# Kernel optimization log

Hardware: AMD Instinct MI355X
Metric: run time of the kernel (lower is better)

## Reference

```python
import jax, jax.numpy as jnp
import numpy as np

C = 512        # concept_num
D = 256        # input_dim / embedding_dim
H = 512        # msg_hidden_dim
M = 256        # msg_output_dim
OH = 512       # hidden_dim
T = 2          # edge_type_num
E = C * (C - 1)  # fully-connected graph without self-loops = 261632


def _glorot(key, shape, fan_in):
    return jax.random.normal(key, shape, jnp.float32) / np.sqrt(fan_in).astype(np.float32)


def setup_inputs() -> dict:
    key = jax.random.key(0)
    ks = jax.random.split(key, 12)
    inputs = jax.random.normal(ks[0], (C, D), jnp.float32)
    rel_type = jax.random.uniform(ks[1], (E, T), jnp.float32)
    send_idx = jax.random.randint(ks[2], (E,), 0, C, jnp.int32)
    rec_idx = jax.random.randint(ks[3], (E,), 0, C, jnp.int32)
    # per-edge-type message MLP params, stacked over type dim
    W1 = _glorot(ks[4], (T, 2 * D, H), 2 * D)
    b1 = jnp.zeros((T, H), jnp.float32)
    W2 = _glorot(ks[5], (T, H, M), H)
    b2 = jnp.zeros((T, M), jnp.float32)
    # output MLP params
    Wo1 = _glorot(ks[6], (M, OH), M)
    bo1 = jnp.zeros((OH,), jnp.float32)
    Wo2 = _glorot(ks[7], (OH, OH), OH)
    bo2 = jnp.zeros((OH,), jnp.float32)
    Wo3 = _glorot(ks[8], (OH, D), OH)
    bo3 = jnp.zeros((D,), jnp.float32)
    return {"inputs": inputs, "rel_type": rel_type, "W1": W1, "b1": b1,
            "W2": W2, "b2": b2, "Wo1": Wo1, "bo1": bo1, "Wo2": Wo2,
            "bo2": bo2, "Wo3": Wo3, "bo3": bo3,
            "send_idx": send_idx, "rec_idx": rec_idx}


def reference(inputs, rel_type, W1, b1, W2, b2, Wo1, bo1, Wo2, bo2, Wo3, bo3,
              send_idx, rec_idx):
    # node2edge: one-hot sparse matmul == index gather
    senders = jnp.take(inputs, send_idx, axis=0)      # [E, D]
    receivers = jnp.take(inputs, rec_idx, axis=0)     # [E, D]
    pre_msg = jnp.concatenate([senders, receivers], axis=-1)  # [E, 2D]
    # per-edge-type MLPs, weighted-summed by rel_type (dropout=0 / eval mode)
    all_msgs = jnp.zeros((pre_msg.shape[0], M), jnp.float32)
    for i in range(T):
        msg = jax.nn.relu(pre_msg @ W1[i] + b1[i])    # [E, H]
        msg = jax.nn.relu(msg @ W2[i] + b2[i])        # [E, M]
        all_msgs = all_msgs + msg * rel_type[:, i:i + 1]
    # edge2node: transposed one-hot sparse matmul == scatter-add over receivers
    agg_msgs = jax.ops.segment_sum(all_msgs, rec_idx, num_segments=inputs.shape[0])  # [C, M]
    pred = jax.nn.relu(agg_msgs @ Wo1 + bo1)
    pred = jax.nn.relu(pred @ Wo2 + bo2)
    return pred @ Wo3 + bo3                           # [C, D]
```

## Files before the change

kernel.cpp:

```cpp
#include <hip/hip_runtime.h>

#define C_N   512
#define E_N   261632
#define CAP   768

typedef _Float16 f16;
typedef _Float16 f16x8_t __attribute__((ext_vector_type(8)));
typedef float    f32x16_t __attribute__((ext_vector_type(16)));

__global__ __launch_bounds__(256) void k_prep_all(
    const float* __restrict__ inputs, const float* __restrict__ W1,
    const float* __restrict__ b1, const float* __restrict__ W2,
    const float* __restrict__ Wo1, const float* __restrict__ Wo2, const float* __restrict__ Wo3,
    f16* __restrict__ SA, f16* __restrict__ RB, f16* __restrict__ W2p,
    f16* __restrict__ Wo1p, f16* __restrict__ Wo2p, f16* __restrict__ Wo3p,
    int* __restrict__ cnt)
{
  __shared__ f16 wt[2][256][18];
  int bid = blockIdx.x;
  int tid = threadIdx.x;
  if (bid < 64) {
    int lane = tid & 63, w = tid >> 6;
    int hlf = lane >> 5, l31 = lane & 31;
    int br = bid & 7, bc = (bid >> 3) & 1, mi = bid >> 4;
    int t = mi >> 1, half = mi & 1;
    const float* Wsrc = W1 + (size_t)t * 512 * 512 + (size_t)half * 256 * 512;

    f32x16_t acc[2][2];
    #pragma unroll
    for (int rt = 0; rt < 2; rt++)
      #pragma unroll
      for (int ctl = 0; ctl < 2; ctl++)
        #pragma unroll
        for (int r = 0; r < 16; r++) acc[rt][ctl][r] = 0.f;

    #pragma unroll
    for (int i = 0; i < 4; i++) {
      int idx = tid + i * 256;
      int k = idx >> 6, n4 = idx & 63;
      float4 v = *(const float4*)&Wsrc[(size_t)k * 512 + bc * 256 + n4 * 4];
      wt[0][n4 * 4 + 0][k] = (f16)v.x;
      wt[0][n4 * 4 + 1][k] = (f16)v.y;
      wt[0][n4 * 4 + 2][k] = (f16)v.z;
      wt[0][n4 * 4 + 3][k] = (f16)v.w;
    }

    for (int kc = 0; kc < 16; kc++) {
      __syncthreads();
      if (kc + 1 < 16) {
        int b = (kc + 1) & 1;
        #pragma unroll
        for (int i = 0; i < 4; i++) {
          int idx = tid + i * 256;
          int k = idx >> 6, n4 = idx & 63;
          float4 v = *(const float4*)&Wsrc[(size_t)((kc + 1) * 16 + k) * 512 + bc * 256 + n4 * 4];
          wt[b][n4 * 4 + 0][k] = (f16)v.x;
          wt[b][n4 * 4 + 1][k] = (f16)v.y;
          wt[b][n4 * 4 + 2][k] = (f16)v.z;
          wt[b][n4 * 4 + 3][k] = (f16)v.w;
        }
      }
      f16x8_t af[2];
      #pragma unroll
      for (int rt = 0; rt < 2; rt++) {
        const float4* p = (const float4*)&inputs[(size_t)(br * 64 + rt * 32 + l31) * 256 + kc * 16 + hlf * 8];
        float4 u0 = p[0], u1 = p[1];
        af[rt] = (f16x8_t){(f16)u0.x, (f16)u0.y, (f16)u0.z, (f16)u0.w,
                           (f16)u1.x, (f16)u1.y, (f16)u1.z, (f16)u1.w};
      }
      int b = kc & 1;
      #pragma unroll
      for (int ctl = 0; ctl < 2; ctl++) {
        int n = (2 * w + ctl) * 32 + l31;
        f16x8_t bfr = *(const f16x8_t*)&wt[b][n][hlf * 8];
        #pragma unroll
        for (int rt = 0; rt < 2; rt++)
          acc[rt][ctl] = __builtin_amdgcn_mfma_f32_32x32x16_f16(af[rt], bfr, acc[rt][ctl], 0, 0, 0);
      }
    }
    f16* dst = (half == 0) ? SA : RB;
    #pragma unroll
    for (int ctl = 0; ctl < 2; ctl++) {
      int col = bc * 256 + (2 * w + ctl) * 32 + l31;
      float bias = (half == 1) ? b1[t * 512 + col] : 0.f;
      #pragma unroll
      for (int rt = 0; rt < 2; rt++)
        #pragma unroll
        for (int r = 0; r < 16; r++) {
          int row = br * 64 + rt * 32 + (r & 3) + 8 * (r >> 2) + 4 * hlf;
          dst[((size_t)(t * 512 + row)) * 512 + col] = (f16)(acc[rt][ctl][r] + bias);
        }
    }
  } else if (bid < 192) {
    int gid  = (bid - 64) * 256 + tid;
    int lane = gid & 63;
    int ct   = (gid >> 6) & 7;
    int kc   = (gid >> 9) & 31;
    int t    = gid >> 14;
    int n    = ct * 32 + (lane & 31);
    int k0   = kc * 16 + (lane >> 5) * 8;
    const float* src = W2 + (size_t)t * 512 * 256;
    f16x8_t v;
    #pragma unroll
    for (int j = 0; j < 8; j++) v[j] = (f16)src[(size_t)(k0 + j) * 256 + n];
    *(f16x8_t*)(W2p + (size_t)gid * 8) = v;
  } else if (bid < 256) {
    int gid  = (bid - 192) * 256 + tid;
    int lane = gid & 63;
    int ct   = (gid >> 6) & 15;
    int kc   = gid >> 10;
    int n    = ct * 32 + (lane & 31);
    int k0   = kc * 16 + (lane >> 5) * 8;
    f16x8_t v;
    #pragma unroll
    for (int j = 0; j < 8; j++) v[j] = (f16)Wo1[(size_t)(k0 + j) * 512 + n];
    *(f16x8_t*)(Wo1p + (size_t)gid * 8) = v;
  } else if (bid < 384) {
    int gid  = (bid - 256) * 256 + tid;
    int lane = gid & 63;
    int ct   = (gid >> 6) & 15;
    int kc   = gid >> 10;
    int n    = ct * 32 + (lane & 31);
    int k0   = kc * 16 + (lane >> 5) * 8;
    f16x8_t v;
    #pragma unroll
    for (int j = 0; j < 8; j++) v[j] = (f16)Wo2[(size_t)(k0 + j) * 512 + n];
    *(f16x8_t*)(Wo2p + (size_t)gid * 8) = v;
  } else if (bid < 448) {
    int gid  = (bid - 384) * 256 + tid;
    int lane = gid & 63;
    int ct   = (gid >> 6) & 7;
    int kc   = gid >> 9;
    int n    = ct * 32 + (lane & 31);
    int k0   = kc * 16 + (lane >> 5) * 8;
    f16x8_t v;
    #pragma unroll
    for (int j = 0; j < 8; j++) v[j] = (f16)Wo3[(size_t)(k0 + j) * 256 + n];
    *(f16x8_t*)(Wo3p + (size_t)gid * 8) = v;
  } else {
    for (int i = tid; i < 512 * 16; i += 256) cnt[i] = 0;
  }
}

__global__ __launch_bounds__(1024) void k_scatter_d(const int* __restrict__ rec,
    const int* __restrict__ send, const float* __restrict__ rel,
    int* __restrict__ cnt, uint2* __restrict__ smeta)
{
  __shared__ int lh[512];
  __shared__ int lb[512];
  int b = blockIdx.x;
  int e0 = b * (E_N / 64);
  if (threadIdx.x < 512) lh[threadIdx.x] = 0;
  __syncthreads();
  for (int i = threadIdx.x; i < E_N / 64; i += 1024)
    atomicAdd(&lh[rec[e0 + i]], 1);
  __syncthreads();
  if (threadIdx.x < 512) {
    int c = lh[threadIdx.x];
    lb[threadIdx.x] = c ? atomicAdd(&cnt[threadIdx.x * 16], c) : 0;
    lh[threadIdx.x] = 0;
  }
  __syncthreads();
  for (int i = threadIdx.x; i < E_N / 64; i += 1024) {
    int e = e0 + i;
    int r = rec[e];
    int p = r * CAP + lb[r] + atomicAdd(&lh[r], 1);
    f16 r0 = (f16)rel[2 * (size_t)e];
    f16 r1 = (f16)rel[2 * (size_t)e + 1];
    unsigned pk = ((unsigned)__builtin_bit_cast(unsigned short, r1) << 16)
                |  (unsigned)__builtin_bit_cast(unsigned short, r0);
    smeta[p] = make_uint2((unsigned)send[e], pk);
  }
}

#define H1S2 264

__global__ __launch_bounds__(512, 4) void k_edges(
    const f16* __restrict__ SA, const f16* __restrict__ RB,
    const f16* __restrict__ W2p, const float* __restrict__ b2,
    const uint2* __restrict__ smeta, const int* __restrict__ cnt,
    float* __restrict__ agg)
{
  __shared__ f16   h1[128 * H1S2];
  __shared__ f16   rbs[2][512];
  __shared__ float b2s[2][256];
  __shared__ float aggL[256];
  __shared__ float relv2[2][128][2];
  __shared__ int   sends2[2][128];

  int c    = blockIdx.x;
  int tid  = threadIdx.x;
  int lane = tid & 63;
  int w    = tid >> 6;
  int hlf  = lane >> 5;
  int l31  = lane & 31;
  int q5   = tid & 31;
  int rb0  = tid >> 5;

  if (tid < 128) {
    int t = tid >> 6, qq = tid & 63;
    *(f16x8_t*)&rbs[t][qq * 8] = *(const f16x8_t*)&RB[((size_t)(t * 512 + c)) * 512 + qq * 8];
  }
  if (tid < 256) aggL[tid] = 0.0f;
  { int t = (tid >> 8) & 1, col = tid & 255; b2s[t][col] = b2[t * 256 + col]; }

  int s0 = c * CAP;
  int s1 = s0 + cnt[c * 16];
  int nt = (s1 - s0 + 127) >> 7;

  if (nt > 0 && tid < 128) {
    int pos = s0 + tid;
    if (pos < s1) {
      uint2 m = smeta[pos];
      sends2[0][tid] = (int)m.x;
      relv2[0][tid][0] = (float)__builtin_bit_cast(f16, (unsigned short)(m.y & 0xffffu));
      relv2[0][tid][1] = (float)__builtin_bit_cast(f16, (unsigned short)(m.y >> 16));
    } else {
      sends2[0][tid] = 0; relv2[0][tid][0] = 0.f; relv2[0][tid][1] = 0.f;
    }
  }
  __syncthreads();

  f16x8_t g[8];
  const f16x8_t* SAc = (const f16x8_t*)SA;
  const f16x8_t* Bp  = (const f16x8_t*)W2p;
  f32x16_t acc[4];

  if (nt > 0) {
    #pragma unroll
    for (int j = 0; j < 8; j++)
      g[j] = SAc[(size_t)sends2[0][rb0 + 16 * j] * 64 + q5];
  }

  for (int ph = 0; ph < 4 * nt; ph++) {
    int ti  = ph >> 2;
    int t   = (ph >> 1) & 1;
    int kh  = ph & 1;
    int cb  = ti & 1;
    int nb  = cb ^ 1;
    bool more = (ti + 1 < nt);

    {
      f16x8_t rbq = *(const f16x8_t*)&rbs[t][(kh * 32 + q5) * 8];
      #pragma unroll
      for (int j = 0; j < 8; j++) {
        int row = rb0 + 16 * j;
        f16x8_t hv;
        #pragma unroll
        for (int e = 0; e < 8; e++) {
          f16 v = (f16)(g[j][e] + rbq[e]);
          hv[e] = (v > (f16)0.0f) ? v : (f16)0.0f;
        }
        *(f16x8_t*)&h1[row * H1S2 + q5 * 8] = hv;
      }
    }
    __syncthreads();

    if (t == 0 && kh == 0 && more && tid < 128) {
      int pos = s0 + (ti + 1) * 128 + tid;
      if (pos < s1) {
        uint2 m = smeta[pos];
        sends2[nb][tid] = (int)m.x;
        relv2[nb][tid][0] = (float)__builtin_bit_cast(f16, (unsigned short)(m.y & 0xffffu));
        relv2[nb][tid][1] = (float)__builtin_bit_cast(f16, (unsigned short)(m.y >> 16));
      } else {
        sends2[nb][tid] = 0; relv2[nb][tid][0] = 0.f; relv2[nb][tid][1] = 0.f;
      }
    }

    if (kh == 0) {
      #pragma unroll
      for (int rt = 0; rt < 4; rt++)
        #pragma unroll
        for (int r = 0; r < 16; r++) acc[rt][r] = 0.f;
    }

    f16x8_t bb[2];
    bb[0] = Bp[(size_t)(((t * 32 + kh * 16 + 0) * 8 + w) * 64 + lane)];
    bb[1] = Bp[(size_t)(((t * 32 + kh * 16 + 1) * 8 + w) * 64 + lane)];

    if (kh == 0) {
      #pragma unroll
      for (int j = 0; j < 8; j++)
        g[j] = SAc[(size_t)(t * 512 + sends2[cb][rb0 + 16 * j]) * 64 + 32 + q5];
    } else if (t == 0) {
      #pragma unroll
      for (int j = 0; j < 8; j++)
        g[j] = SAc[(size_t)(512 + sends2[cb][rb0 + 16 * j]) * 64 + q5];
    } else if (more) {
      #pragma unroll
      for (int j = 0; j < 8; j++)
        g[j] = SAc[(size_t)sends2[nb][rb0 + 16 * j] * 64 + q5];
    }

    for (int kc = 0; kc < 16; kc++) {
      int pb = kc & 1;
      #pragma unroll
      for (int rt = 0; rt < 4; rt++) {
        f16x8_t af = *(const f16x8_t*)&h1[(rt * 32 + l31) * H1S2 + kc * 16 + hlf * 8];
        acc[rt] = __builtin_amdgcn_mfma_f32_32x32x16_f16(af, bb[pb], acc[rt], 0, 0, 0);
      }
      if (kc + 2 < 16)
        bb[pb] = Bp[(size_t)(((t * 32 + kh * 16 + kc + 2) * 8 + w) * 64 + lane)];
    }

    if (kh == 1) {
      int col = w * 32 + l31;
      float b2c = b2s[t][col];
      float csum = 0.0f;
      #pragma unroll
      for (int rt = 0; rt < 4; rt++)
        #pragma unroll
        for (int r = 0; r < 16; r++) {
          int row = rt * 32 + (r & 3) + 8 * (r >> 2) + 4 * hlf;
          float v = fmaxf(acc[rt][r] + b2c, 0.0f);
          csum += v * relv2[cb][row][t];
        }
      csum += __shfl_xor(csum, 32, 64);
      if (hlf == 0) aggL[col] += csum;
    }
    __syncthreads();
  }

  if (tid < 256) agg[(size_t)c * 256 + tid] = aggL[tid];
}

#define HOS 520

__global__ __launch_bounds__(512, 1) void k_omlp(const float* __restrict__ agg,
    const f16* __restrict__ Wo1p, const float* __restrict__ bo1,
    const f16* __restrict__ Wo2p, const float* __restrict__ bo2,
    const f16* __restrict__ Wo3p, const float* __restrict__ bo3,
    float* __restrict__ out)
{
  __shared__ f16 hL1[64 * HOS];
  __shared__ f16 hL2[64 * HOS];
  int tid = threadIdx.x, lane = tid & 63, w = tid >> 6;
  int hlf = lane >> 5, l31 = lane & 31;
  int br = blockIdx.x;

  {
    f32x16_t acc[2][2];
    #pragma unroll
    for (int rt = 0; rt < 2; rt++)
      #pragma unroll
      for (int ctl = 0; ctl < 2; ctl++)
        #pragma unroll
        for (int r = 0; r < 16; r++) acc[rt][ctl][r] = 0.f;
    for (int kc = 0; kc < 16; kc++) {
      f16x8_t af[2];
      #pragma unroll
      for (int rt = 0; rt < 2; rt++) {
        const float4* p = (const float4*)&agg[(size_t)(br * 64 + rt * 32 + l31) * 256 + kc * 16 + hlf * 8];
        float4 u0 = p[0], u1 = p[1];
        af[rt] = (f16x8_t){(f16)u0.x, (f16)u0.y, (f16)u0.z, (f16)u0.w,
                           (f16)u1.x, (f16)u1.y, (f16)u1.z, (f16)u1.w};
      }
      #pragma unroll
      for (int ctl = 0; ctl < 2; ctl++) {
        int ct = 2 * w + ctl;
        f16x8_t bfr = *(const f16x8_t*)&Wo1p[((size_t)(kc * 16 + ct) * 64 + lane) * 8];
        #pragma unroll
        for (int rt = 0; rt < 2; rt++)
          acc[rt][ctl] = __builtin_amdgcn_mfma_f32_32x32x16_f16(af[rt], bfr, acc[rt][ctl], 0, 0, 0);
      }
    }
    #pragma unroll
    for (int ctl = 0; ctl < 2; ctl++) {
      int col = (2 * w + ctl) * 32 + l31;
      float bias = bo1[col];
      #pragma unroll
      for (int rt = 0; rt < 2; rt++)
        #pragma unroll
        for (int r = 0; r < 16; r++) {
          int row = rt * 32 + (r & 3) + 8 * (r >> 2) + 4 * hlf;
          hL1[row * HOS + col] = (f16)fmaxf(acc[rt][ctl][r] + bias, 0.f);
        }
    }
  }
  __syncthreads();

  {
    f32x16_t acc[2][2];
    #pragma unroll
    for (int rt = 0; rt < 2; rt++)
      #pragma unroll
      for (int ctl = 0; ctl < 2; ctl++)
        #pragma unroll
        for (int r = 0; r < 16; r++) acc[rt][ctl][r] = 0.f;
    for (int kc = 0; kc < 32; kc++) {
      f16x8_t af[2];
      #pragma unroll
      for (int rt = 0; rt < 2; rt++)
        af[rt] = *(const f16x8_t*)&hL1[(rt * 32 + l31) * HOS + kc * 16 + hlf * 8];
      #pragma unroll
      for (int ctl = 0; ctl < 2; ctl++) {
        int ct = 2 * w + ctl;
        f16x8_t bfr = *(const f16x8_t*)&Wo2p[((size_t)(kc * 16 + ct) * 64 + lane) * 8];
        #pragma unroll
        for (int rt = 0; rt < 2; rt++)
          acc[rt][ctl] = __builtin_amdgcn_mfma_f32_32x32x16_f16(af[rt], bfr, acc[rt][ctl], 0, 0, 0);
      }
    }
    #pragma unroll
    for (int ctl = 0; ctl < 2; ctl++) {
      int col = (2 * w + ctl) * 32 + l31;
      float bias = bo2[col];
      #pragma unroll
      for (int rt = 0; rt < 2; rt++)
        #pragma unroll
        for (int r = 0; r < 16; r++) {
          int row = rt * 32 + (r & 3) + 8 * (r >> 2) + 4 * hlf;
          hL2[row * HOS + col] = (f16)fmaxf(acc[rt][ctl][r] + bias, 0.f);
        }
    }
  }
  __syncthreads();

  {
    f32x16_t acc[2];
    #pragma unroll
    for (int rt = 0; rt < 2; rt++)
      #pragma unroll
      for (int r = 0; r < 16; r++) acc[rt][r] = 0.f;
    for (int kc = 0; kc < 32; kc++) {
      f16x8_t bfr = *(const f16x8_t*)&Wo3p[((size_t)(kc * 8 + w) * 64 + lane) * 8];
      #pragma unroll
      for (int rt = 0; rt < 2; rt++) {
        f16x8_t af = *(const f16x8_t*)&hL2[(rt * 32 + l31) * HOS + kc * 16 + hlf * 8];
        acc[rt] = __builtin_amdgcn_mfma_f32_32x32x16_f16(af, bfr, acc[rt], 0, 0, 0);
      }
    }
    int col = w * 32 + l31;
    float bias = bo3[col];
    #pragma unroll
    for (int rt = 0; rt < 2; rt++)
      #pragma unroll
      for (int r = 0; r < 16; r++) {
        int row = br * 64 + rt * 32 + (r & 3) + 8 * (r >> 2) + 4 * hlf;
        out[(size_t)row * 256 + col] = acc[rt][r] + bias;
      }
  }
}

extern "C" void kernel_launch(void* const* d_in, const int* in_sizes, int n_in,
                              void* d_out, int out_size, void* d_ws, size_t ws_size,
                              hipStream_t stream)
{
  (void)in_sizes; (void)n_in; (void)out_size; (void)ws_size;
  const float* inputs = (const float*)d_in[0];
  const float* rel    = (const float*)d_in[1];
  const float* W1     = (const float*)d_in[2];
  const float* b1     = (const float*)d_in[3];
  const float* W2     = (const float*)d_in[4];
  const float* b2     = (const float*)d_in[5];
  const float* Wo1    = (const float*)d_in[6];
  const float* bo1    = (const float*)d_in[7];
  const float* Wo2    = (const float*)d_in[8];
  const float* bo2    = (const float*)d_in[9];
  const float* Wo3    = (const float*)d_in[10];
  const float* bo3    = (const float*)d_in[11];
  const int* send_idx = (const int*)d_in[12];
  const int* rec_idx  = (const int*)d_in[13];
  float* out = (float*)d_out;

  char* ws = (char*)d_ws;
  f16*    SA    = (f16*)   (ws);
  f16*    RB    = (f16*)   (ws + (1024u << 10));
  f16*    W2p   = (f16*)   (ws + (2048u << 10));
  float*  agg   = (float*) (ws + (2560u << 10));
  int*    cnt   = (int*)   (ws + (3072u << 10));
  f16*    Wo1p  = (f16*)   (ws + (3136u << 10));
  f16*    Wo2p  = (f16*)   (ws + (3392u << 10));
  f16*    Wo3p  = (f16*)   (ws + (3904u << 10));
  uint2*  smeta = (uint2*) (ws + (4160u << 10));

  k_prep_all <<<dim3(449), dim3(256),  0, stream>>>(inputs, W1, b1, W2, Wo1, Wo2, Wo3,
                                                    SA, RB, W2p, Wo1p, Wo2p, Wo3p, cnt);
  k_scatter_d<<<dim3(64),  dim3(1024), 0, stream>>>(rec_idx, send_idx, rel, cnt, smeta);
  k_edges    <<<dim3(512), dim3(512),  0, stream>>>(SA, RB, W2p, b2, smeta, cnt, agg);
  k_omlp     <<<dim3(8),   dim3(512),  0, stream>>>(agg, Wo1p, bo1, Wo2p, bo2, Wo3p, bo3, out);
}
```

Before: 309.5 us.

## Split edge tiles across a 2D grid with atomic aggregation, widen scatter and output MLP grids

The edge kernel now launches one block per (receiver, 128-edge tile) on a 512x5 grid instead of looping over every tile of a receiver inside one block. Partial sums are combined with atomicAdd into agg, which the prep kernel now zeroes in an extra block. This spreads work over more blocks and removes imbalance from receivers with many edges, at the cost of reloading RB and b2 per tile, extra atomics, and empty blocks that exit early. The scatter kernel uses 128 blocks of 512 threads, and the output MLP uses 16 blocks of 32 rows each, to raise parallelism in both.

After: 298.9 us, median of 2. -3.4%, faster.

```diff
diff --git a/kernel.cpp b/kernel.cpp
--- a/kernel.cpp
+++ b/kernel.cpp
@@ -14,7 +14,7 @@
     const float* __restrict__ Wo1, const float* __restrict__ Wo2, const float* __restrict__ Wo3,
     f16* __restrict__ SA, f16* __restrict__ RB, f16* __restrict__ W2p,
     f16* __restrict__ Wo1p, f16* __restrict__ Wo2p, f16* __restrict__ Wo3p,
-    int* __restrict__ cnt)
+    int* __restrict__ cnt, float* __restrict__ agg)
 {
   __shared__ f16 wt[2][256][18];
   int bid = blockIdx.x;
@@ -137,31 +137,34 @@
     #pragma unroll
     for (int j = 0; j < 8; j++) v[j] = (f16)Wo3[(size_t)(k0 + j) * 256 + n];
     *(f16x8_t*)(Wo3p + (size_t)gid * 8) = v;
+  } else if (bid == 448) {
+    for (int i = tid; i < 512 * 16; i += 256) cnt[i] = 0;
   } else {
-    for (int i = tid; i < 512 * 16; i += 256) cnt[i] = 0;
+    float4* a4 = (float4*)agg;
+    for (int i = tid; i < 512 * 64; i += 256) a4[i] = make_float4(0.f, 0.f, 0.f, 0.f);
   }
 }
 
-__global__ __launch_bounds__(1024) void k_scatter_d(const int* __restrict__ rec,
+__global__ __launch_bounds__(512) void k_scatter_d(const int* __restrict__ rec,
     const int* __restrict__ send, const float* __restrict__ rel,
     int* __restrict__ cnt, uint2* __restrict__ smeta)
 {
   __shared__ int lh[512];
   __shared__ int lb[512];
   int b = blockIdx.x;
-  int e0 = b * (E_N / 64);
-  if (threadIdx.x < 512) lh[threadIdx.x] = 0;
-  __syncthreads();
-  for (int i = threadIdx.x; i < E_N / 64; i += 1024)
+  int e0 = b * (E_N / 128);
+  lh[threadIdx.x] = 0;
+  __syncthreads();
+  for (int i = threadIdx.x; i < E_N / 128; i += 512)
     atomicAdd(&lh[rec[e0 + i]], 1);
   __syncthreads();
-  if (threadIdx.x < 512) {
+  {
     int c = lh[threadIdx.x];
     lb[threadIdx.x] = c ? atomicAdd(&cnt[threadIdx.x * 16], c) : 0;
     lh[threadIdx.x] = 0;
   }
   __syncthreads();
-  for (int i = threadIdx.x; i < E_N / 64; i += 1024) {
+  for (int i = threadIdx.x; i < E_N / 128; i += 512) {
     int e = e0 + i;
     int r = rec[e];
     int p = r * CAP + lb[r] + atomicAdd(&lh[r], 1);
@@ -185,10 +188,14 @@
   __shared__ f16   rbs[2][512];
   __shared__ float b2s[2][256];
   __shared__ float aggL[256];
-  __shared__ float relv2[2][128][2];
-  __shared__ int   sends2[2][128];
-
-  int c    = blockIdx.x;
+  __shared__ float relv[128][2];
+  __shared__ int   sends[128];
+
+  int c   = blockIdx.x;
+  int ti  = blockIdx.y;
+  int n_c = cnt[c * 16];
+  if (ti * 128 >= n_c) return;
+
   int tid  = threadIdx.x;
   int lane = tid & 63;
   int w    = tid >> 6;
@@ -204,19 +211,17 @@
   if (tid < 256) aggL[tid] = 0.0f;
   { int t = (tid >> 8) & 1, col = tid & 255; b2s[t][col] = b2[t * 256 + col]; }
 
-  int s0 = c * CAP;
-  int s1 = s0 + cnt[c * 16];
-  int nt = (s1 - s0 + 127) >> 7;
-
-  if (nt > 0 && tid < 128) {
-    int pos = s0 + tid;
-    if (pos < s1) {
-      uint2 m = smeta[pos];
-      sends2[0][tid] = (int)m.x;
-      relv2[0][tid][0] = (float)__builtin_bit_cast(f16, (unsigned short)(m.y & 0xffffu));
-      relv2[0][tid][1] = (float)__builtin_bit_cast(f16, (unsigned short)(m.y >> 16));
+  int s0 = c * CAP + ti * 128;
+  int nv = n_c - ti * 128; if (nv > 128) nv = 128;
+
+  if (tid < 128) {
+    if (tid < nv) {
+      uint2 m = smeta[s0 + tid];
+      sends[tid] = (int)m.x;
+      relv[tid][0] = (float)__builtin_bit_cast(f16, (unsigned short)(m.y & 0xffffu));
+      relv[tid][1] = (float)__builtin_bit_cast(f16, (unsigned short)(m.y >> 16));
     } else {
-      sends2[0][tid] = 0; relv2[0][tid][0] = 0.f; relv2[0][tid][1] = 0.f;
+      sends[tid] = 0; relv[tid][0] = 0.f; relv[tid][1] = 0.f;
     }
   }
   __syncthreads();
@@ -226,19 +231,13 @@
   const f16x8_t* Bp  = (const f16x8_t*)W2p;
   f32x16_t acc[4];
 
-  if (nt > 0) {
-    #pragma unroll
-    for (int j = 0; j < 8; j++)
-      g[j] = SAc[(size_t)sends2[0][rb0 + 16 * j] * 64 + q5];
-  }
-
-  for (int ph = 0; ph < 4 * nt; ph++) {
-    int ti  = ph >> 2;
-    int t   = (ph >> 1) & 1;
-    int kh  = ph & 1;
-    int cb  = ti & 1;
-    int nb  = cb ^ 1;
-    bool more = (ti + 1 < nt);
+  #pragma unroll
+  for (int j = 0; j < 8; j++)
+    g[j] = SAc[(size_t)sends[rb0 + 16 * j] * 64 + q5];
+
+  for (int ph = 0; ph < 4; ph++) {
+    int t  = ph >> 1;
+    int kh = ph & 1;
 
     {
       f16x8_t rbq = *(const f16x8_t*)&rbs[t][(kh * 32 + q5) * 8];
@@ -256,18 +255,6 @@
     }
     __syncthreads();
 
-    if (t == 0 && kh == 0 && more && tid < 128) {
-      int pos = s0 + (ti + 1) * 128 + tid;
-      if (pos < s1) {
-        uint2 m = smeta[pos];
-        sends2[nb][tid] = (int)m.x;
-        relv2[nb][tid][0] = (float)__builtin_bit_cast(f16, (unsigned short)(m.y & 0xffffu));
-        relv2[nb][tid][1] = (float)__builtin_bit_cast(f16, (unsigned short)(m.y >> 16));
-      } else {
-        sends2[nb][tid] = 0; relv2[nb][tid][0] = 0.f; relv2[nb][tid][1] = 0.f;
-      }
-    }
-
     if (kh == 0) {
       #pragma unroll
       for (int rt = 0; rt < 4; rt++)
@@ -279,18 +266,12 @@
     bb[0] = Bp[(size_t)(((t * 32 + kh * 16 + 0) * 8 + w) * 64 + lane)];
     bb[1] = Bp[(size_t)(((t * 32 + kh * 16 + 1) * 8 + w) * 64 + lane)];
 
-    if (kh == 0) {
+    if (ph < 3) {
+      int tn  = (ph + 1) >> 1;
+      int khn = (ph + 1) & 1;
       #pragma unroll
       for (int j = 0; j < 8; j++)
-        g[j] = SAc[(size_t)(t * 512 + sends2[cb][rb0 + 16 * j]) * 64 + 32 + q5];
-    } else if (t == 0) {
-      #pragma unroll
-      for (int j = 0; j < 8; j++)
-        g[j] = SAc[(size_t)(512 + sends2[cb][rb0 + 16 * j]) * 64 + q5];
-    } else if (more) {
-      #pragma unroll
-      for (int j = 0; j < 8; j++)
-        g[j] = SAc[(size_t)sends2[nb][rb0 + 16 * j] * 64 + q5];
+        g[j] = SAc[(size_t)(tn * 512 + sends[rb0 + 16 * j]) * 64 + khn * 32 + q5];
     }
 
     for (int kc = 0; kc < 16; kc++) {
@@ -314,7 +295,7 @@
         for (int r = 0; r < 16; r++) {
           int row = rt * 32 + (r & 3) + 8 * (r >> 2) + 4 * hlf;
           float v = fmaxf(acc[rt][r] + b2c, 0.0f);
-          csum += v * relv2[cb][row][t];
+          csum += v * relv[row][t];
         }
       csum += __shfl_xor(csum, 32, 64);
       if (hlf == 0) aggL[col] += csum;
@@ -322,7 +303,7 @@
     __syncthreads();
   }
 
-  if (tid < 256) agg[(size_t)c * 256 + tid] = aggL[tid];
+  if (tid < 256) atomicAdd(&agg[(size_t)c * 256 + tid], aggL[tid]);
 }
 
 #define HOS 520
@@ -333,36 +314,28 @@
     const f16* __restrict__ Wo3p, const float* __restrict__ bo3,
     float* __restrict__ out)
 {
-  __shared__ f16 hL1[64 * HOS];
-  __shared__ f16 hL2[64 * HOS];
+  __shared__ f16 hL1[32 * HOS];
+  __shared__ f16 hL2[32 * HOS];
   int tid = threadIdx.x, lane = tid & 63, w = tid >> 6;
   int hlf = lane >> 5, l31 = lane & 31;
   int br = blockIdx.x;
 
   {
-    f32x16_t acc[2][2];
-    #pragma unroll
-    for (int rt = 0; rt < 2; rt++)
-      #pragma unroll
-      for (int ctl = 0; ctl < 2; ctl++)
-        #pragma unroll
-        for (int r = 0; r < 16; r++) acc[rt][ctl][r] = 0.f;
+    f32x16_t acc[2];
+    #pragma unroll
+    for (int ctl = 0; ctl < 2; ctl++)
+      #pragma unroll
+      for (int r = 0; r < 16; r++) acc[ctl][r] = 0.f;
     for (int kc = 0; kc < 16; kc++) {
-      f16x8_t af[2];
-      #pragma unroll
-      for (int rt = 0; rt < 2; rt++) {
-        const float4* p = (const float4*)&agg[(size_t)(br * 64 + rt * 32 + l31) * 256 + kc * 16 + hlf * 8];
-        float4 u0 = p[0], u1 = p[1];
-        af[rt] = (f16x8_t){(f16)u0.x, (f16)u0.y, (f16)u0.z, (f16)u0.w,
-                           (f16)u1.x, (f16)u1.y, (f16)u1.z, (f16)u1.w};
-      }
+      const float4* p = (const float4*)&agg[(size_t)(br * 32 + l31) * 256 + kc * 16 + hlf * 8];
+      float4 u0 = p[0], u1 = p[1];
+      f16x8_t af = (f16x8_t){(f16)u0.x, (f16)u0.y, (f16)u0.z, (f16)u0.w,
+                             (f16)u1.x, (f16)u1.y, (f16)u1.z, (f16)u1.w};
       #pragma unroll
       for (int ctl = 0; ctl < 2; ctl++) {
         int ct = 2 * w + ctl;
         f16x8_t bfr = *(const f16x8_t*)&Wo1p[((size_t)(kc * 16 + ct) * 64 + lane) * 8];
-        #pragma unroll
-        for (int rt = 0; rt < 2; rt++)
-          acc[rt][ctl] = __builtin_amdgcn_mfma_f32_32x32x16_f16(af[rt], bfr, acc[rt][ctl], 0, 0, 0);
+        acc[ctl] = __builtin_amdgcn_mfma_f32_32x32x16_f16(af, bfr, acc[ctl], 0, 0, 0);
       }
     }
     #pragma unroll
@@ -370,36 +343,27 @@
       int col = (2 * w + ctl) * 32 + l31;
       float bias = bo1[col];
       #pragma unroll
-      for (int rt = 0; rt < 2; rt++)
-        #pragma unroll
-        for (int r = 0; r < 16; r++) {
-          int row = rt * 32 + (r & 3) + 8 * (r >> 2) + 4 * hlf;
-          hL1[row * HOS + col] = (f16)fmaxf(acc[rt][ctl][r] + bias, 0.f);
-        }
+      for (int r = 0; r < 16; r++) {
+        int row = (r & 3) + 8 * (r >> 2) + 4 * hlf;
+        hL1[row * HOS + col] = (f16)fmaxf(acc[ctl][r] + bias, 0.f);
+      }
     }
   }
   __syncthreads();
 
   {
-    f32x16_t acc[2][2];
-    #pragma unroll
-    for (int rt = 0; rt < 2; rt++)
-      #pragma unroll
-      for (int ctl = 0; ctl < 2; ctl++)
-        #pragma unroll
-        for (int r = 0; r < 16; r++) acc[rt][ctl][r] = 0.f;
+    f32x16_t acc[2];
+    #pragma unroll
+    for (int ctl = 0; ctl < 2; ctl++)
+      #pragma unroll
+      for (int r = 0; r < 16; r++) acc[ctl][r] = 0.f;
     for (int kc = 0; kc < 32; kc++) {
-      f16x8_t af[2];
-      #pragma unroll
-      for (int rt = 0; rt < 2; rt++)
-        af[rt] = *(const f16x8_t*)&hL1[(rt * 32 + l31) * HOS + kc * 16 + hlf * 8];
+      f16x8_t af = *(const f16x8_t*)&hL1[l31 * HOS + kc * 16 + hlf * 8];
       #pragma unroll
       for (int ctl = 0; ctl < 2; ctl++) {
         int ct = 2 * w + ctl;
         f16x8_t bfr = *(const f16x8_t*)&Wo2p[((size_t)(kc * 16 + ct) * 64 + lane) * 8];
-        #pragma unroll
-        for (int rt = 0; rt < 2; rt++)
-          acc[rt][ctl] = __builtin_amdgcn_mfma_f32_32x32x16_f16(af[rt], bfr, acc[rt][ctl], 0, 0, 0);
+        acc[ctl] = __builtin_amdgcn_mfma_f32_32x32x16_f16(af, bfr, acc[ctl], 0, 0, 0);
       }
     }
     #pragma unroll
@@ -407,39 +371,30 @@
       int col = (2 * w + ctl) * 32 + l31;
       float bias = bo2[col];
       #pragma unroll
-      for (int rt = 0; rt < 2; rt++)
-        #pragma unroll
-        for (int r = 0; r < 16; r++) {
-          int row = rt * 32 + (r & 3) + 8 * (r >> 2) + 4 * hlf;
-          hL2[row * HOS + col] = (f16)fmaxf(acc[rt][ctl][r] + bias, 0.f);
-        }
+      for (int r = 0; r < 16; r++) {
+        int row = (r & 3) + 8 * (r >> 2) + 4 * hlf;
+        hL2[row * HOS + col] = (f16)fmaxf(acc[ctl][r] + bias, 0.f);
+      }
     }
   }
   __syncthreads();
 
   {
-    f32x16_t acc[2];
-    #pragma unroll
-    for (int rt = 0; rt < 2; rt++)
-      #pragma unroll
-      for (int r = 0; r < 16; r++) acc[rt][r] = 0.f;
+    f32x16_t acc;
+    #pragma unroll
+    for (int r = 0; r < 16; r++) acc[r] = 0.f;
     for (int kc = 0; kc < 32; kc++) {
+      f16x8_t af  = *(const f16x8_t*)&hL2[l31 * HOS + kc * 16 + hlf * 8];
       f16x8_t bfr = *(const f16x8_t*)&Wo3p[((size_t)(kc * 8 + w) * 64 + lane) * 8];
-      #pragma unroll
-      for (int rt = 0; rt < 2; rt++) {
-        f16x8_t af = *(const f16x8_t*)&hL2[(rt * 32 + l31) * HOS + kc * 16 + hlf * 8];
-        acc[rt] = __builtin_amdgcn_mfma_f32_32x32x16_f16(af, bfr, acc[rt], 0, 0, 0);
-      }
+      acc = __builtin_amdgcn_mfma_f32_32x32x16_f16(af, bfr, acc, 0, 0, 0);
     }
     int col = w * 32 + l31;
     float bias = bo3[col];
     #pragma unroll
-    for (int rt = 0; rt < 2; rt++)
-      #pragma unroll
-      for (int r = 0; r < 16; r++) {
-        int row = br * 64 + rt * 32 + (r & 3) + 8 * (r >> 2) + 4 * hlf;
-        out[(size_t)row * 256 + col] = acc[rt][r] + bias;
-      }
+    for (int r = 0; r < 16; r++) {
+      int row = br * 32 + (r & 3) + 8 * (r >> 2) + 4 * hlf;
+      out[(size_t)row * 256 + col] = acc[r] + bias;
+    }
   }
 }
 
@@ -475,9 +430,9 @@
   f16*    Wo3p  = (f16*)   (ws + (3904u << 10));
   uint2*  smeta = (uint2*) (ws + (4160u << 10));
 
-  k_prep_all <<<dim3(449), dim3(256),  0, stream>>>(inputs, W1, b1, W2, Wo1, Wo2, Wo3,
-                                                    SA, RB, W2p, Wo1p, Wo2p, Wo3p, cnt);
-  k_scatter_d<<<dim3(64),  dim3(1024), 0, stream>>>(rec_idx, send_idx, rel, cnt, smeta);
-  k_edges    <<<dim3(512), dim3(512),  0, stream>>>(SA, RB, W2p, b2, smeta, cnt, agg);
-  k_omlp     <<<dim3(8),   dim3(512),  0, stream>>>(agg, Wo1p, bo1, Wo2p, bo2, Wo3p, bo3, out);
+  k_prep_all <<<dim3(450),    dim3(256), 0, stream>>>(inputs, W1, b1, W2, Wo1, Wo2, Wo3,
+                                                      SA, RB, W2p, Wo1p, Wo2p, Wo3p, cnt, agg);
+  k_scatter_d<<<dim3(128),    dim3(512), 0, stream>>>(rec_idx, send_idx, rel, cnt, smeta);
+  k_edges    <<<dim3(512, 5), dim3(512), 0, stream>>>(SA, RB, W2p, b2, smeta, cnt, agg);
+  k_omlp     <<<dim3(16),     dim3(512), 0, stream>>>(agg, Wo1p, bo1, Wo2p, bo2, Wo3p, bo3, out);
 }
```
